# Kernel tuning notes

Hardware: AMD Instinct MI355X
Metric: run time of the kernel (lower is better)

The kernel has to match this reference:

```python
import jax, jax.numpy as jnp
import numpy as np

R = 4                      # search_range
D = 2 * R + 1              # 9 -> 81 cost channels
FILTERS = [128, 128, 96, 64, 32, 2]


def mish(x):
    return x * jnp.tanh(jax.nn.softplus(x))


def sep_conv(x, dw, pw, b, act):
    # depthwise 3x3 (depth_multiplier=1), then pointwise 1x1, bias after pointwise
    y = jax.lax.conv_general_dilated(
        x, dw, window_strides=(1, 1), padding='SAME',
        dimension_numbers=('NHWC', 'HWIO', 'NHWC'),
        feature_group_count=x.shape[-1])
    y = jax.lax.conv_general_dilated(
        y, pw, window_strides=(1, 1), padding='SAME',
        dimension_numbers=('NHWC', 'HWIO', 'NHWC'))
    if b is not None:
        y = y + b
    return mish(y) if act else y


def cost_volume(prv, nxt):
    B, H, W, C = prv.shape
    pad = jnp.pad(nxt, ((0, 0), (R, R), (R, R), (0, 0)))
    # (2R+1)^2 shifted correlations, mean over channels (matches tf.reduce_mean axis=3)
    costs = [jnp.mean(prv * pad[:, i:i + H, j:j + W, :], axis=3)
             for i in range(D) for j in range(D)]
    return jnp.stack(costs, axis=3)  # [B,H,W,81]


def setup_inputs() -> dict:
    key = jax.random.key(0)
    ks = jax.random.split(key, 40)
    B, H, W, C = 8, 128, 128, 128
    inp = {
        'prv': jax.random.normal(ks[0], (B, H, W, C), jnp.float32),
        'nxt': jax.random.normal(ks[1], (B, H, W, C), jnp.float32),
    }
    in_ch = [D * D + 2 * C] + FILTERS[:-1]  # [337,128,128,96,64,32]
    ki = 2
    for i, (ci, f) in enumerate(zip(in_ch, FILTERS)):
        inp[f'dw{i}'] = jax.random.normal(ks[ki], (3, 3, 1, ci), jnp.float32) * 0.05; ki += 1
        inp[f'pw{i}'] = jax.random.normal(ks[ki], (1, 1, ci, f), jnp.float32) * 0.05; ki += 1
        if i < len(FILTERS) - 1:  # last layer: use_bias=False
            inp[f'b{i}'] = jnp.zeros((f,), jnp.float32)
    return inp


def reference(prv, nxt,
              dw0, pw0, b0, dw1, pw1, b1, dw2, pw2, b2,
              dw3, pw3, b3, dw4, pw4, b4, dw5, pw5):
    cost = cost_volume(prv, nxt)
    x = jnp.concatenate([cost, prv, nxt], axis=-1)
    x = sep_conv(x, dw0, pw0, b0, True)
    x = sep_conv(x, dw1, pw1, b1, True)
    x = sep_conv(x, dw2, pw2, b2, True)
    x = sep_conv(x, dw3, pw3, b3, True)
    x = sep_conv(x, dw4, pw4, b4, True)
    x = sep_conv(x, dw5, pw5, None, False)  # flow head: no bias, no activation
    return x
```

## Files before the change

kernel.cpp:

```cpp
#include <hip/hip_runtime.h>
#include <math.h>

#define BATCH 8
#define HH 128
#define WW 128
#define CC 128
#define RR 4
#define DDIM 9
#define NS 81
#define NSP 96
#define HWPIX (HH*WW)
#define DSLAB 1032

typedef short  short8  __attribute__((ext_vector_type(8)));
typedef float  f32x4   __attribute__((ext_vector_type(4)));

__device__ __forceinline__ short bf16h(float f){
    unsigned u = __float_as_uint(f);
    u += 0x7fffu + ((u >> 16) & 1u);
    return (short)(u >> 16);
}
__device__ __forceinline__ float bf16f(short s){
    return __uint_as_float(((unsigned)(unsigned short)s) << 16);
}
__device__ __forceinline__ float mish_f(float x){
    float xc = fminf(x, 30.f);
    float t = expf(xc);
    float u = t*t + 2.f*t;
    return x * (u / (u + 2.f));
}

__device__ __forceinline__ void gld16(float* lds, const float* g){
    __builtin_amdgcn_global_load_lds(
        (const __attribute__((address_space(1))) unsigned int*)g,
        (__attribute__((address_space(3))) unsigned int*)lds, 16, 0, 0);
}

__device__ __forceinline__ void lds_barrier(){
    __asm volatile("s_waitcnt lgkmcnt(0)\n\ts_barrier" ::: "memory");
}

__global__ void zero_k(float* p, int n){
    int i = blockIdx.x*256 + threadIdx.x;
    if(i < n) p[i] = 0.f;
}

__device__ __forceinline__ void cvt8(const float4& a, const float4& b,
                                     short8& h, short8& l){
    float v0=a.x,v1=a.y,v2=a.z,v3=a.w,v4=b.x,v5=b.y,v6=b.z,v7=b.w;
    short h0=bf16h(v0),h1=bf16h(v1),h2=bf16h(v2),h3=bf16h(v3);
    short h4=bf16h(v4),h5=bf16h(v5),h6=bf16h(v6),h7=bf16h(v7);
    h[0]=h0;h[1]=h1;h[2]=h2;h[3]=h3;h[4]=h4;h[5]=h5;h[6]=h6;h[7]=h7;
    l[0]=bf16h(v0-bf16f(h0)); l[1]=bf16h(v1-bf16f(h1));
    l[2]=bf16h(v2-bf16f(h2)); l[3]=bf16h(v3-bf16f(h3));
    l[4]=bf16h(v4-bf16f(h4)); l[5]=bf16h(v5-bf16f(h5));
    l[6]=bf16h(v6-bf16f(h6)); l[7]=bf16h(v7-bf16f(h7));
}

__global__ __launch_bounds__(512,2) void cost_mfma(
    const float* __restrict__ prv, const float* __restrict__ nxt,
    float* __restrict__ cost)
{
    __shared__ char smem[73728];
    short* bhs = (short*)smem;
    short* bls = (short*)(smem + 36864);
    const int tid  = threadIdx.x;
    const int lane = tid & 63, wv = tid >> 6;
    const int l15  = lane & 15, quad = lane >> 4;
    const int x0 = blockIdx.x*16, y0 = blockIdx.y*16, b = blockIdx.z;
    const int Y = wv*2;

    const float* prvb = prv + (((size_t)b*HH + y0)*WW + x0)*CC;
    const float* nxb  = nxt + (size_t)b*HH*WW*CC;

    f32x4 acc[2][9][2];
#pragma unroll
    for(int yy=0;yy<2;yy++)
#pragma unroll
        for(int i=0;i<9;i++){
            acc[yy][i][0] = (f32x4){0.f,0.f,0.f,0.f};
            acc[yy][i][1] = (f32x4){0.f,0.f,0.f,0.f};
        }

    float4 sreg[9];
    auto sload = [&](int kc){
#pragma unroll
        for(int s=0;s<9;s++){
            int e = s*512 + tid;
            int px = e >> 3, q = e & 7;
            int r = px/24, c = px - r*24;
            int hy = y0 - 4 + r, hx = x0 - 4 + c;
            bool ok = hy>=0 && hy<HH && hx>=0 && hx<WW;
            sreg[s] = ok ? *(const float4*)(nxb + ((size_t)hy*WW + hx)*CC + kc*32 + q*4)
                         : make_float4(0.f,0.f,0.f,0.f);
        }
    };
    sload(0);

    for(int kc=0; kc<4; kc++){
        __syncthreads();
#pragma unroll
        for(int s=0;s<9;s++){
            int e = s*512 + tid;
            int px = e >> 3, q = e & 7;
            int r = px/24, c = px - r*24;
            int base = ((r*4 + (q>>1))*24 + c)*8 + (q&1)*4;
            float4 v = sreg[s];
            short h0=bf16h(v.x), h1=bf16h(v.y), h2=bf16h(v.z), h3=bf16h(v.w);
            *(short4*)&bhs[base] = make_short4(h0,h1,h2,h3);
            *(short4*)&bls[base] = make_short4(bf16h(v.x-bf16f(h0)),
                                               bf16h(v.y-bf16f(h1)),
                                               bf16h(v.z-bf16f(h2)),
                                               bf16h(v.w-bf16f(h3)));
        }
        if(kc < 3) sload(kc+1);
        short8 Ah[2], Al[2];
#pragma unroll
        for(int yy=0; yy<2; yy++){
            const float* ap = prvb + ((size_t)(Y+yy)*WW + l15)*CC + kc*32 + quad*8;
            float4 f0v = *(const float4*)ap;
            float4 f1v = *(const float4*)(ap+4);
            cvt8(f0v, f1v, Ah[yy], Al[yy]);
        }
        lds_barrier();
#pragma unroll
        for(int rr=0; rr<10; rr++){
            int r  = Y + rr;
            int rb = (r*4 + quad)*24*8;
            short8 Bh0 = *(const short8*)&bhs[rb + l15*8];
            short8 Bl0 = *(const short8*)&bls[rb + l15*8];
            short8 Bh1 = *(const short8*)&bhs[rb + (8+l15)*8];
            short8 Bl1 = *(const short8*)&bls[rb + (8+l15)*8];
#pragma unroll
            for(int yy=0; yy<2; yy++){
                int i = rr - yy;
                if(i >= 0 && i <= 8){
                    f32x4 c0 = acc[yy][i][0];
                    c0 = __builtin_amdgcn_mfma_f32_16x16x32_bf16(Ah[yy],Bh0,c0,0,0,0);
                    c0 = __builtin_amdgcn_mfma_f32_16x16x32_bf16(Al[yy],Bh0,c0,0,0,0);
                    c0 = __builtin_amdgcn_mfma_f32_16x16x32_bf16(Ah[yy],Bl0,c0,0,0,0);
                    c0 = __builtin_amdgcn_mfma_f32_16x16x32_bf16(Al[yy],Bl0,c0,0,0,0);
                    acc[yy][i][0] = c0;
                    f32x4 c1 = acc[yy][i][1];
                    c1 = __builtin_amdgcn_mfma_f32_16x16x32_bf16(Ah[yy],Bh1,c1,0,0,0);
                    c1 = __builtin_amdgcn_mfma_f32_16x16x32_bf16(Al[yy],Bh1,c1,0,0,0);
                    c1 = __builtin_amdgcn_mfma_f32_16x16x32_bf16(Ah[yy],Bl1,c1,0,0,0);
                    c1 = __builtin_amdgcn_mfma_f32_16x16x32_bf16(Al[yy],Bl1,c1,0,0,0);
                    acc[yy][i][1] = c1;
                }
            }
        }
    }
    const float sc = 1.f/128.f;
    float* obuf = (float*)smem;
    const int grp = wv >> 2;
#pragma unroll
    for(int p=0; p<2; p++){
        lds_barrier();
        if(grp == p){
#pragma unroll
            for(int yy=0; yy<2; yy++){
                int rl = (Y + yy - p*8)*16;
#pragma unroll
                for(int i=0;i<9;i++){
#pragma unroll
                    for(int rg=0; rg<4; rg++){
                        int m  = quad*4 + rg;
                        int j0 = l15 - m;
                        if(j0 >= 0 && j0 <= 8)
                            obuf[(rl + m)*96 + i*9 + j0] = acc[yy][i][0][rg]*sc;
                        int j1 = 8 + l15 - m;
                        if(l15 >= 8 && j1 <= 8)
                            obuf[(rl + m)*96 + i*9 + j1] = acc[yy][i][1][rg]*sc;
                    }
                }
            }
        }
        for(int e = tid; e < 1920; e += 512){
            int px = e/15, c = e - px*15;
            obuf[px*96 + 81 + c] = 0.f;
        }
        lds_barrier();
        float* gbase = cost + (((size_t)b*HH + y0 + p*8)*WW + x0)*NSP;
#pragma unroll
        for(int it=0; it<6; it++){
            int e = it*512 + tid;
            int r = e/384, o = e - r*384;
            float4 v = *(const float4*)&obuf[r*1536 + o*4];
            *(float4*)&gbase[(size_t)r*WW*NSP + o*4] = v;
        }
    }
}

__global__ void prep_pw(const float* __restrict__ src, short* __restrict__ dh,
                        short* __restrict__ dl, int K, int N, int NP, int total,
                        int remap)
{
    int idx = blockIdx.x*256 + threadIdx.x;
    if(idx >= total) return;
    int j  = idx & 7;
    int n  = (idx>>3) % NP;
    int k8 = (idx>>3) / NP;
    int k  = k8*8 + j;
    if(remap) k = (k < 81) ? k : ((k < 96) ? -1 : k - 15);
    float v = (k>=0 && k<K && n<N) ? src[(size_t)k*N + n] : 0.f;
    short h = bf16h(v);
    dh[idx] = h;
    dl[idx] = bf16h(v - bf16f(h));
}

__global__ void prep_dw(const float* __restrict__ src, float* __restrict__ dst,
                        int K, int K0, int remap, int total)
{
    int idx = blockIdx.x*256 + threadIdx.x;
    if(idx >= total) return;
    int k = idx / K0, c = idx - k*K0;
    int cr = c;
    if(remap) cr = (c < 81) ? c : ((c < 96) ? -1 : c - 15);
    dst[idx] = (cr>=0 && cr<K) ? src[k*K + cr] : 0.f;
}

template<int CINR,int K0,int COUT,int NP,bool BIAS,bool ACT,bool CONCAT>
__global__ __launch_bounds__(256,2) void sep_mfma(
    const float* __restrict__ xin, const float* __restrict__ cost,
    const float* __restrict__ prv, const float* __restrict__ nxt,
    const float* __restrict__ dwp, const short* __restrict__ wh,
    const short* __restrict__ wl, const float* __restrict__ bias,
    const float* __restrict__ zb, float* __restrict__ out)
{
    constexpr int TN = NP/32;
    __shared__ float xs[2][180*36];
    __shared__ short dshh[4*DSLAB];
    __shared__ short dshl[4*DSLAB];
    __shared__ float dwls[2][9*32];

    const int tid = threadIdx.x;
    const int x0 = blockIdx.x*16, y0 = blockIdx.y*8, b = blockIdx.z;
    const int lane = tid & 63;
    const int wv   = tid >> 6;
    const int wm   = wv >> 1, wn = wv & 1;
    const int l15  = lane & 15, quad = lane >> 4;

    f32x4 acc[4][TN];
#pragma unroll
    for(int i=0;i<4;i++)
#pragma unroll
        for(int nt=0;nt<TN;nt++) acc[i][nt] = (f32x4){0.f,0.f,0.f,0.f};

    auto stage = [&](int c0, int pb){
        if(tid < 72)
            gld16(&dwls[pb][(tid>>3)*32 + (tid&7)*4],
                  dwp + (tid>>3)*K0 + c0 + (tid&7)*4);
        const float* src; int str, coff;
        if(CONCAT){
            if(c0 < 96)      { src = cost; str = NSP; coff = c0; }
            else if(c0 < 224){ src = prv;  str = 128; coff = c0-96; }
            else             { src = nxt;  str = 128; coff = c0-224; }
        } else { src = xin; str = CINR; coff = c0; }
        const float* sb = src + (size_t)b*HH*WW*str + coff;
        float* xp = &xs[pb][0];
#pragma unroll
        for(int it=0;it<7;it++){
            int e = it*256 + tid;
            if(e < 1620){
                int hp = e/9, q = e - hp*9;
                int hy = y0-1 + hp/18, hx = x0-1 + hp%18;
                bool ok = (q < 8) && hy>=0 && hy<HH && hx>=0 && hx<WW;
                const float* gp = ok ? (sb + ((size_t)hy*WW + hx)*str + q*4)
                                     : zb;
                gld16(xp + hp*36 + q*4, gp);
            }
        }
    };

    const int c4  = tid & 7;
    const int pxg = tid >> 3;
    const int dpy = pxg >> 2;
    const int dxb = (pxg & 3) * 4;

    stage(0, 0);
    int pb = 0;
    for(int c0=0;c0<K0;c0+=32){
        __syncthreads();
        const int k8 = (c0>>3) + quad;
        short8 Bh[TN], Bl[TN];
#pragma unroll
        for(int nt=0;nt<TN;nt++){
            int n = wn*(NP/2) + nt*16 + l15;
            size_t off = ((size_t)k8*NP + n)*8;
            Bh[nt] = *(const short8*)(wh + off);
            Bl[nt] = *(const short8*)(wl + off);
        }
        if(c0+32 < K0) stage(c0+32, pb^1);
        const float* xp = &xs[pb][0];
        const float* dwc = &dwls[pb][0];
        {
            float4 o[4];
#pragma unroll
            for(int dx=0;dx<4;dx++) o[dx] = make_float4(0.f,0.f,0.f,0.f);
#pragma unroll
            for(int kh=0;kh<3;kh++){
                float4 xw[6];
#pragma unroll
                for(int t=0;t<6;t++)
                    xw[t] = *(const float4*)&xp[((dpy+kh)*18 + dxb + t)*36 + c4*4];
#pragma unroll
                for(int kw=0;kw<3;kw++){
                    float4 w4 = *(const float4*)&dwc[(kh*3+kw)*32 + c4*4];
#pragma unroll
                    for(int dx=0;dx<4;dx++){
                        float4 xv = xw[kw+dx];
                        o[dx].x = fmaf(xv.x,w4.x,o[dx].x);
                        o[dx].y = fmaf(xv.y,w4.y,o[dx].y);
                        o[dx].z = fmaf(xv.z,w4.z,o[dx].z);
                        o[dx].w = fmaf(xv.w,w4.w,o[dx].w);
                    }
                }
            }
            const int wbase = (c4>>1)*DSLAB + (pxg*4)*8 + (c4&1)*4;
#pragma unroll
            for(int dx=0;dx<4;dx++){
                float4 s = o[dx];
                short h0=bf16h(s.x), h1=bf16h(s.y), h2=bf16h(s.z), h3=bf16h(s.w);
                short l0=bf16h(s.x-bf16f(h0)), l1=bf16h(s.y-bf16f(h1));
                short l2=bf16h(s.z-bf16f(h2)), l3=bf16h(s.w-bf16f(h3));
                *(short4*)&dshh[wbase + dx*8] = make_short4(h0,h1,h2,h3);
                *(short4*)&dshl[wbase + dx*8] = make_short4(l0,l1,l2,l3);
            }
        }
        lds_barrier();
#pragma unroll
        for(int i=0;i<4;i++){
            int ab = quad*DSLAB + (wm*64 + i*16 + l15)*8;
            short8 Ah = *(const short8*)&dshh[ab];
            short8 Al = *(const short8*)&dshl[ab];
#pragma unroll
            for(int nt=0;nt<TN;nt++){
                f32x4 c = acc[i][nt];
                c = __builtin_amdgcn_mfma_f32_16x16x32_bf16(Ah,Bh[nt],c,0,0,0);
                c = __builtin_amdgcn_mfma_f32_16x16x32_bf16(Al,Bh[nt],c,0,0,0);
                c = __builtin_amdgcn_mfma_f32_16x16x32_bf16(Ah,Bl[nt],c,0,0,0);
                acc[i][nt] = c;
            }
        }
        lds_barrier();
        pb ^= 1;
    }
#pragma unroll
    for(int i=0;i<4;i++){
        int pxb = wm*64 + i*16 + quad*4;
#pragma unroll
        for(int nt=0;nt<TN;nt++){
            int cout = wn*(NP/2) + nt*16 + l15;
            if(cout < COUT){
                float bv = BIAS ? bias[cout] : 0.f;
#pragma unroll
                for(int r=0;r<4;r++){
                    int p = pxb + r;
                    int y = y0 + (p>>4), x = x0 + (p&15);
                    float v = acc[i][nt][r] + bv;
                    if(ACT) v = mish_f(v);
                    out[(((size_t)b*HH + y)*WW + x)*COUT + cout] = v;
                }
            }
        }
    }
}

extern "C" void kernel_launch(void* const* d_in, const int* in_sizes, int n_in,
                              void* d_out, int out_size, void* d_ws, size_t ws_size,
                              hipStream_t stream)
{
    (void)in_sizes; (void)n_in; (void)out_size;
    const float* prv = (const float*)d_in[0];
    const float* nxt = (const float*)d_in[1];
    const float* dws[6] = {(const float*)d_in[2],(const float*)d_in[5],(const float*)d_in[8],
                           (const float*)d_in[11],(const float*)d_in[14],(const float*)d_in[17]};
    const float* pws[6] = {(const float*)d_in[3],(const float*)d_in[6],(const float*)d_in[9],
                           (const float*)d_in[12],(const float*)d_in[15],(const float*)d_in[18]};
    const float* b0  = (const float*)d_in[4];
    const float* b1  = (const float*)d_in[7];
    const float* b2  = (const float*)d_in[10];
    const float* b3  = (const float*)d_in[13];
    const float* b4  = (const float*)d_in[16];

    const int   Ks[6]   = {337,128,128, 96, 64, 32};
    const int   K0s[6]  = {352,128,128, 96, 64, 32};
    const int   Ns[6]   = {128,128, 96, 64, 32,  2};
    const int   NPs[6]  = {128,128, 96, 64, 32, 32};
    const int   rmp[6]  = {  1,  0,  0,  0,  0,  0};
    size_t offs[6]; size_t E = 0;
    for(int i=0;i<6;i++){ offs[i] = E; E += (size_t)K0s[i]*NPs[i]; }
    size_t dwoffs[6]; size_t Edw = 0;
    for(int i=0;i<6;i++){ dwoffs[i] = Edw; Edw += (size_t)9*K0s[i]; }

    short* Whs = (short*)d_ws;
    short* Wls = Whs + E;
    float* Dwp = (float*)((char*)d_ws + ((E*2*sizeof(short) + 255) & ~(size_t)255));
    float* Zb  = Dwp + Edw;
    size_t wbytes = (((char*)(Zb + 64) - (char*)d_ws) + 255) & ~(size_t)255;

    zero_k<<<1,64,0,stream>>>(Zb, 64);
    for(int i=0;i<6;i++){
        int total = K0s[i]*NPs[i];
        prep_pw<<<(total+255)/256,256,0,stream>>>(pws[i], Whs+offs[i], Wls+offs[i],
                                                  Ks[i], Ns[i], NPs[i], total, rmp[i]);
        int tdw = 9*K0s[i];
        prep_dw<<<(tdw+255)/256,256,0,stream>>>(dws[i], Dwp+dwoffs[i],
                                                Ks[i], K0s[i], rmp[i], tdw);
    }

    const size_t per_batch_floats = (size_t)HWPIX * (NSP + 128 + 128);
    size_t avail = (ws_size > wbytes) ? (ws_size - wbytes) : 0;
    int NB = (int)(avail / (per_batch_floats * sizeof(float)));
    if(NB > BATCH) NB = BATCH;
    if(NB < 1)     NB = 1;
    while(BATCH % NB) NB--;

    float* fbase = (float*)((char*)d_ws + wbytes);
    float* costb = fbase;
    float* bufA  = costb + (size_t)NB*HWPIX*NSP;
    float* bufB  = bufA  + (size_t)NB*HWPIX*128;

    for(int bb=0; bb<BATCH; bb+=NB){
        const float* prv_o = prv + (size_t)bb*HWPIX*CC;
        const float* nxt_o = nxt + (size_t)bb*HWPIX*CC;
        float*       out_o = (float*)d_out + (size_t)bb*HWPIX*2;
        dim3 gc(WW/16, HH/16, NB);
        dim3 gs(WW/16, HH/8,  NB);

        cost_mfma<<<gc,512,0,stream>>>(prv_o, nxt_o, costb);
        sep_mfma<337,352,128,128,true ,true ,true ><<<gs,256,0,stream>>>(nullptr, costb, prv_o, nxt_o, Dwp+dwoffs[0], Whs+offs[0], Wls+offs[0], b0, Zb, bufA);
        sep_mfma<128,128,128,128,true ,true ,false><<<gs,256,0,stream>>>(bufA, nullptr,nullptr,nullptr, Dwp+dwoffs[1], Whs+offs[1], Wls+offs[1], b1, Zb, bufB);
        sep_mfma<128,128, 96, 96,true ,true ,false><<<gs,256,0,stream>>>(bufB, nullptr,nullptr,nullptr, Dwp+dwoffs[2], Whs+offs[2], Wls+offs[2], b2, Zb, bufA);
        sep_mfma< 96, 96, 64, 64,true ,true ,false><<<gs,256,0,stream>>>(bufA, nullptr,nullptr,nullptr, Dwp+dwoffs[3], Whs+offs[3], Wls+offs[3], b3, Zb, bufB);
        sep_mfma< 64, 64, 32, 32,true ,true ,false><<<gs,256,0,stream>>>(bufB, nullptr,nullptr,nullptr, Dwp+dwoffs[4], Whs+offs[4], Wls+offs[4], b4, Zb, bufA);
        sep_mfma< 32, 32,  2, 32,false,false,false><<<gs,256,0,stream>>>(bufA, nullptr,nullptr,nullptr, Dwp+dwoffs[5], Whs+offs[5], Wls+offs[5], nullptr, Zb, out_o);
    }
}
```

Before: 574.5 us.

## Double-buffer cost-volume LDS tiles and pad LDS strides against bank conflicts

The cost-volume MFMA kernel now keeps two LDS buffers for the bf16 hi/lo split of the `nxt` halo tile. The next channel chunk is converted and written into the idle buffer after the MFMAs on the current one. This drops the per-iteration `__syncthreads` plus store-then-compute serialisation and moves the global prefetch two chunks ahead. The LDS row stride is padded from 24 to 25 groups and the output staging stride from 96 to 100 floats, to reduce bank conflicts. In exchange LDS use grows to 150 KB per block, so only one 512-thread block fits per CU instead of two, which halves resident waves and may offset the overlap gain.

```diff
diff --git a/kernel.cpp b/kernel.cpp
--- a/kernel.cpp
+++ b/kernel.cpp
@@ -11,6 +11,8 @@
 #define NSP 96
 #define HWPIX (HH*WW)
 #define DSLAB 1032
+#define GSTR 25
+#define BSLAB 19200
 
 typedef short  short8  __attribute__((ext_vector_type(8)));
 typedef float  f32x4   __attribute__((ext_vector_type(4)));
@@ -61,9 +63,7 @@
     const float* __restrict__ prv, const float* __restrict__ nxt,
     float* __restrict__ cost)
 {
-    __shared__ char smem[73728];
-    short* bhs = (short*)smem;
-    short* bls = (short*)(smem + 36864);
+    __shared__ __align__(16) char smem[153600];
     const int tid  = threadIdx.x;
     const int lane = tid & 63, wv = tid >> 6;
     const int l15  = lane & 15, quad = lane >> 4;
@@ -95,16 +95,15 @@
                          : make_float4(0.f,0.f,0.f,0.f);
         }
     };
-    sload(0);
-
-    for(int kc=0; kc<4; kc++){
-        __syncthreads();
+    auto swrite = [&](int p){
+        short* bhs = (short*)(smem + p*76800);
+        short* bls = (short*)(smem + p*76800 + 38400);
 #pragma unroll
         for(int s=0;s<9;s++){
             int e = s*512 + tid;
             int px = e >> 3, q = e & 7;
             int r = px/24, c = px - r*24;
-            int base = ((r*4 + (q>>1))*24 + c)*8 + (q&1)*4;
+            int base = ((r*4 + (q>>1))*GSTR + c)*8 + (q&1)*4;
             float4 v = sreg[s];
             short h0=bf16h(v.x), h1=bf16h(v.y), h2=bf16h(v.z), h3=bf16h(v.w);
             *(short4*)&bhs[base] = make_short4(h0,h1,h2,h3);
@@ -113,20 +112,31 @@
                                                bf16h(v.z-bf16f(h2)),
                                                bf16h(v.w-bf16f(h3)));
         }
-        if(kc < 3) sload(kc+1);
+    };
+
+    sload(0);
+    swrite(0);
+    sload(1);
+
+#pragma unroll
+    for(int kc=0; kc<4; kc++){
+        const int p = kc & 1;
+        const float* ap0 = prvb + ((size_t)(Y+0)*WW + l15)*CC + kc*32 + quad*8;
+        const float* ap1 = prvb + ((size_t)(Y+1)*WW + l15)*CC + kc*32 + quad*8;
+        float4 a00 = *(const float4*)ap0;
+        float4 a01 = *(const float4*)(ap0+4);
+        float4 a10 = *(const float4*)ap1;
+        float4 a11 = *(const float4*)(ap1+4);
+        lds_barrier();
         short8 Ah[2], Al[2];
-#pragma unroll
-        for(int yy=0; yy<2; yy++){
-            const float* ap = prvb + ((size_t)(Y+yy)*WW + l15)*CC + kc*32 + quad*8;
-            float4 f0v = *(const float4*)ap;
-            float4 f1v = *(const float4*)(ap+4);
-            cvt8(f0v, f1v, Ah[yy], Al[yy]);
-        }
-        lds_barrier();
+        cvt8(a00, a01, Ah[0], Al[0]);
+        cvt8(a10, a11, Ah[1], Al[1]);
+        const short* bhs = (const short*)(smem + p*76800);
+        const short* bls = (const short*)(smem + p*76800 + 38400);
 #pragma unroll
         for(int rr=0; rr<10; rr++){
             int r  = Y + rr;
-            int rb = (r*4 + quad)*24*8;
+            int rb = (r*4 + quad)*GSTR*8;
             short8 Bh0 = *(const short8*)&bhs[rb + l15*8];
             short8 Bl0 = *(const short8*)&bls[rb + l15*8];
             short8 Bh1 = *(const short8*)&bhs[rb + (8+l15)*8];
@@ -150,6 +160,10 @@
                 }
             }
         }
+        if(kc < 3){
+            swrite(p^1);
+            if(kc < 2) sload(kc+2);
+        }
     }
     const float sc = 1.f/128.f;
     float* obuf = (float*)smem;
@@ -168,17 +182,17 @@
                         int m  = quad*4 + rg;
                         int j0 = l15 - m;
                         if(j0 >= 0 && j0 <= 8)
-                            obuf[(rl + m)*96 + i*9 + j0] = acc[yy][i][0][rg]*sc;
+                            obuf[(rl + m)*100 + i*9 + j0] = acc[yy][i][0][rg]*sc;
                         int j1 = 8 + l15 - m;
                         if(l15 >= 8 && j1 <= 8)
-                            obuf[(rl + m)*96 + i*9 + j1] = acc[yy][i][1][rg]*sc;
+                            obuf[(rl + m)*100 + i*9 + j1] = acc[yy][i][1][rg]*sc;
                     }
                 }
             }
         }
         for(int e = tid; e < 1920; e += 512){
             int px = e/15, c = e - px*15;
-            obuf[px*96 + 81 + c] = 0.f;
+            obuf[px*100 + 81 + c] = 0.f;
         }
         lds_barrier();
         float* gbase = cost + (((size_t)b*HH + y0 + p*8)*WW + x0)*NSP;
@@ -186,7 +200,8 @@
         for(int it=0; it<6; it++){
             int e = it*512 + tid;
             int r = e/384, o = e - r*384;
-            float4 v = *(const float4*)&obuf[r*1536 + o*4];
+            int px = o/24, c4 = o - px*24;
+            float4 v = *(const float4*)&obuf[(r*16 + px)*100 + c4*4];
             *(float4*)&gbase[(size_t)r*WW*NSP + o*4] = v;
         }
     }
```

Measured after the change: 618.6 us. 1.08x slower.
